# Optimization experiments

Hardware: AMD Instinct MI355X
Metric: run time of the kernel (lower is better)

The kernel has to match this reference:

```python
import jax, jax.numpy as jnp
import numpy as np

B, S, D = 4, 4096, 1024
DFF = 4 * D
ACTIVE = 1024  # ceil(S * 0.25)


def setup_inputs() -> dict:
    key = jax.random.key(0)
    ks = jax.random.split(key, 4)
    x = jax.random.normal(ks[0], (B, S, D), dtype=jnp.float32)
    rw = jax.random.normal(ks[1], (D,), dtype=jnp.float32) * 0.02
    rb = jnp.zeros((1,), dtype=jnp.float32)
    w1 = jax.random.normal(ks[2], (D, DFF), dtype=jnp.float32) * 0.02
    b1 = jnp.zeros((DFF,), dtype=jnp.float32)
    w2 = jax.random.normal(ks[3], (DFF, D), dtype=jnp.float32) * 0.02
    b2 = jnp.zeros((D,), dtype=jnp.float32)
    return {"x": x, "rw": rw, "rb": rb, "w1": w1, "b1": b1,
            "w2": w2, "b2": b2, "active_tokens": ACTIVE}


def reference(x, rw, rb, w1, b1, w2, b2, active_tokens):
    b, s, d = x.shape
    # router: Linear(n_embd, 1) -> [B, S] scores
    scores = jnp.einsum('bsd,d->bs', x, rw) + rb[0]
    # top-k tokens per batch row
    _, idx = jax.lax.top_k(scores, active_tokens)          # [B, K] int32
    sel = jnp.take_along_axis(x, idx[..., None], axis=1)   # [B, K, D]
    # dense MLP on selected tokens (exact GELU as in torch nn.GELU)
    h = jax.nn.gelu(jnp.einsum('bkd,df->bkf', sel, w1) + b1, approximate=False)
    out = jnp.einsum('bkf,fd->bkd', h, w2) + b2            # [B, K, D]
    # sigmoid gate from router scores of selected tokens
    gates = jax.nn.sigmoid(jnp.take_along_axis(scores, idx, axis=1))  # [B, K]
    out = out * gates[..., None]
    # scatter back into zeros at selected positions
    flat_idx = (idx + jnp.arange(b, dtype=idx.dtype)[:, None] * s).reshape(-1)
    flat_out = jnp.zeros((b * s, d), dtype=out.dtype)
    flat_out = flat_out.at[flat_idx].set(out.reshape(-1, d))
    return flat_out.reshape(b, s, d)
```

## Files before the change

### kernel.cpp

```cpp
#include <hip/hip_runtime.h>
#include <hip/hip_bf16.h>
#include <cstdint>
#include <cstddef>

#define Bz 4
#define Sz 4096
#define Dz 1024
#define DFFz 4096
#define KACT 1024

typedef __bf16 bf16;
typedef __attribute__((ext_vector_type(8))) __bf16 bf16x8;
typedef __attribute__((ext_vector_type(4))) __bf16 bf16x4;
typedef __attribute__((ext_vector_type(4))) float f32x4;

__device__ __forceinline__ void async16(const void* g, void* l) {
  __builtin_amdgcn_global_load_lds(
      (const __attribute__((address_space(1))) void*)g,
      (__attribute__((address_space(3))) void*)l, 16, 0, 0);
}

__global__ void router_k(const float* __restrict__ x, const float* __restrict__ rw,
                         const float* __restrict__ rb, float* __restrict__ scores,
                         float4* __restrict__ out4) {
  int row = blockIdx.x * 4 + (threadIdx.x >> 6);
  int lane = threadIdx.x & 63;
  const float4* xr = (const float4*)(x + (size_t)row * Dz);
  const float4* wr = (const float4*)rw;
  float acc = 0.f;
#pragma unroll
  for (int i = 0; i < 4; ++i) {
    float4 a = xr[lane + i * 64];
    float4 w = wr[lane + i * 64];
    acc += a.x * w.x + a.y * w.y + a.z * w.z + a.w * w.w;
  }
#pragma unroll
  for (int d = 32; d; d >>= 1) acc += __shfl_down(acc, d, 64);
  if (lane == 0) scores[row] = acc + rb[0];
  float4* o = out4 + (size_t)blockIdx.x * 4 * (Dz / 4);
  const float4 z = make_float4(0.f, 0.f, 0.f, 0.f);
#pragma unroll
  for (int i = 0; i < 4; ++i) o[threadIdx.x + i * 256] = z;
}

__global__ void transpose_cvt(const float* __restrict__ in, bf16* __restrict__ out,
                              int R, int C) {
  __shared__ float t[32][33];
  int c0 = blockIdx.x * 32, r0 = blockIdx.y * 32;
  int tx = threadIdx.x, ty = threadIdx.y;
#pragma unroll
  for (int i = 0; i < 32; i += 8) t[ty + i][tx] = in[(size_t)(r0 + ty + i) * C + c0 + tx];
  __syncthreads();
#pragma unroll
  for (int i = 0; i < 32; i += 8)
    out[(size_t)(c0 + ty + i) * R + r0 + tx] = (bf16)t[tx][ty + i];
}

__global__ __launch_bounds__(256) void select_gather_k(
    const float* __restrict__ x, const float* __restrict__ scores,
    int* __restrict__ sel_idx, float* __restrict__ gates, bf16* __restrict__ Xsel) {
  int b = blockIdx.x >> 8;
  int s0 = (blockIdx.x & 255) * 16;
  __shared__ float sc[Sz];
  __shared__ int red[16][4];
  __shared__ int rk[16];
  const int tid = threadIdx.x;
  const int wave = tid >> 6, lane = tid & 63;
  const float* srow = scores + (size_t)b * Sz;
#pragma unroll
  for (int i = 0; i < 4; ++i)
    ((float4*)sc)[tid + i * 256] = ((const float4*)srow)[tid + i * 256];
  __syncthreads();
  float mine[16];
#pragma unroll
  for (int j = 0; j < 16; ++j) mine[j] = sc[s0 + j];
  int cnt[16] = {};
  for (int t = tid; t < Sz; t += 256) {
    float o = sc[t];
#pragma unroll
    for (int j = 0; j < 16; ++j)
      cnt[j] += (o > mine[j]) || (o == mine[j] && t < s0 + j);
  }
#pragma unroll
  for (int j = 0; j < 16; ++j) {
    int c = cnt[j];
#pragma unroll
    for (int d = 32; d; d >>= 1) c += __shfl_down(c, d, 64);
    if (lane == 0) red[j][wave] = c;
  }
  __syncthreads();
  if (tid < 16) {
    int rank = red[tid][0] + red[tid][1] + red[tid][2] + red[tid][3];
    rk[tid] = rank;
    if (rank < KACT) {
      int m = b * KACT + rank;
      sel_idx[m] = s0 + tid;
      gates[m] = 1.f / (1.f + expf(-sc[s0 + tid]));
    }
  }
  __syncthreads();
#pragma unroll
  for (int j = 0; j < 16; ++j) {
    int rank = rk[j];
    if (rank >= KACT) continue;
    int m = b * KACT + rank;
    float4 v = ((const float4*)(x + ((size_t)b * Sz + s0 + j) * Dz))[tid];
    bf16x4 o = {(bf16)v.x, (bf16)v.y, (bf16)v.z, (bf16)v.w};
    ((bf16x4*)(Xsel + (size_t)m * Dz))[tid] = o;
  }
}

__global__ __launch_bounds__(256) void gemm1_k(const bf16* __restrict__ A,
                                               const bf16* __restrict__ Bt,
                                               const float* __restrict__ bias,
                                               bf16* __restrict__ H) {
  constexpr int K = Dz, N = DFFz;
  __shared__ __align__(16) bf16 As[128 * 32];
  __shared__ __align__(16) bf16 Bs[128 * 32];
  const int tid = threadIdx.x;
  const int wave = tid >> 6, lane = tid & 63;
  const int quad = lane >> 4, l16 = lane & 15;
  const int m0 = blockIdx.y * 128, n0 = blockIdx.x * 128;
  const int wm = (wave >> 1) * 64, wn = (wave & 1) * 64;
  const int r0 = tid >> 2;
  const int kk = (tid & 3) * 8;

  f32x4 acc[4][4] = {};

  const bf16* Ag = A + (size_t)(m0 + r0) * K + kk;
  const bf16* Bg = Bt + (size_t)(n0 + r0) * K + kk;
  bf16* lAs0 = &As[wave * 512];
  bf16* lAs1 = &As[2048 + wave * 512];
  bf16* lBs0 = &Bs[wave * 512];
  bf16* lBs1 = &Bs[2048 + wave * 512];

  for (int k0 = 0; k0 < K; k0 += 32) {
    async16(Ag + k0, lAs0);
    async16(Ag + (size_t)64 * K + k0, lAs1);
    async16(Bg + k0, lBs0);
    async16(Bg + (size_t)64 * K + k0, lBs1);
    __syncthreads();
    bf16x8 af[4], bfr[4];
#pragma unroll
    for (int i = 0; i < 4; ++i) {
      af[i] = *(const bf16x8*)&As[(wm + i * 16 + l16) * 32 + quad * 8];
      bfr[i] = *(const bf16x8*)&Bs[(wn + i * 16 + l16) * 32 + quad * 8];
    }
#pragma unroll
    for (int mi = 0; mi < 4; ++mi)
#pragma unroll
      for (int ni = 0; ni < 4; ++ni)
        acc[mi][ni] = __builtin_amdgcn_mfma_f32_16x16x32_bf16(af[mi], bfr[ni], acc[mi][ni], 0, 0, 0);
    __syncthreads();
  }

#pragma unroll
  for (int mi = 0; mi < 4; ++mi) {
    int mbase = m0 + wm + mi * 16 + quad * 4;
#pragma unroll
    for (int ni = 0; ni < 4; ++ni) {
      int n = n0 + wn + ni * 16 + l16;
      float bn = bias[n];
#pragma unroll
      for (int r = 0; r < 4; ++r) {
        float z = acc[mi][ni][r] + bn;
        float g = 0.5f * z * (1.f + erff(z * 0.70710678118654752f));
        H[(size_t)(mbase + r) * N + n] = (bf16)g;
      }
    }
  }
}

__global__ __launch_bounds__(256) void gemm2_k(const bf16* __restrict__ A,
                                               const bf16* __restrict__ Bt,
                                               const float* __restrict__ bias,
                                               const int* __restrict__ sel_idx,
                                               const float* __restrict__ gates,
                                               float* __restrict__ out) {
  constexpr int K = DFFz;
  __shared__ __align__(16) bf16 As[128 * 32];
  __shared__ __align__(16) bf16 Bs[64 * 32];
  const int tid = threadIdx.x;
  const int wave = tid >> 6, lane = tid & 63;
  const int quad = lane >> 4, l16 = lane & 15;
  const int m0 = blockIdx.y * 128, n0 = blockIdx.x * 64;
  const int wm = (wave >> 1) * 64, wn = (wave & 1) * 32;
  const int r0 = tid >> 2;
  const int kk = (tid & 3) * 8;

  f32x4 acc[4][2] = {};

  const bf16* Ag = A + (size_t)(m0 + r0) * K + kk;
  const bf16* Bg = Bt + (size_t)(n0 + r0) * K + kk;
  bf16* lAs0 = &As[wave * 512];
  bf16* lAs1 = &As[2048 + wave * 512];
  bf16* lBs0 = &Bs[wave * 512];

  for (int k0 = 0; k0 < K; k0 += 32) {
    async16(Ag + k0, lAs0);
    async16(Ag + (size_t)64 * K + k0, lAs1);
    async16(Bg + k0, lBs0);
    __syncthreads();
    bf16x8 af[4], bfr[2];
#pragma unroll
    for (int i = 0; i < 4; ++i)
      af[i] = *(const bf16x8*)&As[(wm + i * 16 + l16) * 32 + quad * 8];
#pragma unroll
    for (int j = 0; j < 2; ++j)
      bfr[j] = *(const bf16x8*)&Bs[(wn + j * 16 + l16) * 32 + quad * 8];
#pragma unroll
    for (int mi = 0; mi < 4; ++mi)
#pragma unroll
      for (int ni = 0; ni < 2; ++ni)
        acc[mi][ni] = __builtin_amdgcn_mfma_f32_16x16x32_bf16(af[mi], bfr[ni], acc[mi][ni], 0, 0, 0);
    __syncthreads();
  }

#pragma unroll
  for (int mi = 0; mi < 4; ++mi) {
#pragma unroll
    for (int r = 0; r < 4; ++r) {
      int m = m0 + wm + mi * 16 + quad * 4 + r;
      int b = m >> 10;
      int s = sel_idx[m];
      float gt = gates[m];
      float* orow = out + ((size_t)b * Sz + s) * Dz;
#pragma unroll
      for (int ni = 0; ni < 2; ++ni) {
        int n = n0 + wn + ni * 16 + l16;
        orow[n] = (acc[mi][ni][r] + bias[n]) * gt;
      }
    }
  }
}

extern "C" void kernel_launch(void* const* d_in, const int* in_sizes, int n_in,
                              void* d_out, int out_size, void* d_ws, size_t ws_size,
                              hipStream_t stream) {
  (void)in_sizes; (void)n_in; (void)out_size; (void)ws_size;
  const float* x  = (const float*)d_in[0];
  const float* rw = (const float*)d_in[1];
  const float* rb = (const float*)d_in[2];
  const float* w1 = (const float*)d_in[3];
  const float* b1 = (const float*)d_in[4];
  const float* w2 = (const float*)d_in[5];
  const float* b2 = (const float*)d_in[6];
  float* out = (float*)d_out;

  char* ws = (char*)d_ws;
  float* scores = (float*)ws;  ws += (size_t)Bz * Sz * 4;
  int*   sel_idx = (int*)ws;   ws += (size_t)Bz * KACT * 4;
  float* gates = (float*)ws;   ws += (size_t)Bz * KACT * 4;
  bf16*  w1T = (bf16*)ws;      ws += (size_t)DFFz * Dz * 2;
  bf16*  w2T = (bf16*)ws;      ws += (size_t)Dz * DFFz * 2;
  bf16*  Xsel = (bf16*)ws;     ws += (size_t)Bz * KACT * Dz * 2;
  bf16*  H = (bf16*)ws;        ws += (size_t)Bz * KACT * DFFz * 2;

  router_k<<<(Bz * Sz) / 4, 256, 0, stream>>>(x, rw, rb, scores, (float4*)out);
  transpose_cvt<<<dim3(DFFz / 32, Dz / 32), dim3(32, 8), 0, stream>>>(w1, w1T, Dz, DFFz);
  transpose_cvt<<<dim3(Dz / 32, DFFz / 32), dim3(32, 8), 0, stream>>>(w2, w2T, DFFz, Dz);
  select_gather_k<<<Bz * (Sz / 16), 256, 0, stream>>>(x, scores, sel_idx, gates, Xsel);
  gemm1_k<<<dim3(DFFz / 128, (Bz * KACT) / 128), 256, 0, stream>>>(Xsel, w1T, b1, H);
  gemm2_k<<<dim3(Dz / 64, (Bz * KACT) / 128), 256, 0, stream>>>(H, w2T, b2, sel_idx, gates, out);
}
```

Baseline: 315.3 us.

## Use BK=64 double-chunk k-steps and split-K the second GEMM with reduce kernel

Both GEMMs now load two 32-wide k-chunks per barrier pair, halving the number of synchronizations per unit of K. The second GEMM switches from 128x64 to 128x128 tiles and splits K into two halves over a z-grid. It writes bf16 partials into the workspace region reused from w1T. A new reduce kernel sums the two partials, adds bias, applies the gate and scatters rows to the output. This trades an extra kernel launch, extra partial-buffer traffic and bf16 rounding of partials for better occupancy and reuse in gemm2.

```diff
diff --git a/kernel.cpp b/kernel.cpp
--- a/kernel.cpp
+++ b/kernel.cpp
@@ -110,13 +110,38 @@
   }
 }
 
+#define GEMM_BK64_STEP(k0)                                                     \
+  _Pragma("unroll")                                                            \
+  for (int h = 0; h < 2; ++h) {                                                \
+    async16(Ag + (k0) + h * 32, &As[h * 4096 + tid * 8]);                      \
+    async16(Ag + (size_t)64 * K + (k0) + h * 32, &As[h * 4096 + 2048 + tid * 8]); \
+    async16(Bg + (k0) + h * 32, &Bs[h * 4096 + tid * 8]);                      \
+    async16(Bg + (size_t)64 * K + (k0) + h * 32, &Bs[h * 4096 + 2048 + tid * 8]); \
+  }                                                                            \
+  __syncthreads();                                                             \
+  _Pragma("unroll")                                                            \
+  for (int h = 0; h < 2; ++h) {                                                \
+    bf16x8 af[4], bfr[4];                                                      \
+    _Pragma("unroll")                                                          \
+    for (int i = 0; i < 4; ++i) {                                              \
+      af[i] = *(const bf16x8*)&As[h * 4096 + (wm + i * 16 + l16) * 32 + quad * 8]; \
+      bfr[i] = *(const bf16x8*)&Bs[h * 4096 + (wn + i * 16 + l16) * 32 + quad * 8]; \
+    }                                                                          \
+    _Pragma("unroll")                                                          \
+    for (int mi = 0; mi < 4; ++mi)                                             \
+      _Pragma("unroll")                                                        \
+      for (int ni = 0; ni < 4; ++ni)                                           \
+        acc[mi][ni] = __builtin_amdgcn_mfma_f32_16x16x32_bf16(af[mi], bfr[ni], acc[mi][ni], 0, 0, 0); \
+  }                                                                            \
+  __syncthreads();
+
 __global__ __launch_bounds__(256) void gemm1_k(const bf16* __restrict__ A,
                                                const bf16* __restrict__ Bt,
                                                const float* __restrict__ bias,
                                                bf16* __restrict__ H) {
   constexpr int K = Dz, N = DFFz;
-  __shared__ __align__(16) bf16 As[128 * 32];
-  __shared__ __align__(16) bf16 Bs[128 * 32];
+  __shared__ __align__(16) bf16 As[2 * 128 * 32];
+  __shared__ __align__(16) bf16 Bs[2 * 128 * 32];
   const int tid = threadIdx.x;
   const int wave = tid >> 6, lane = tid & 63;
   const int quad = lane >> 4, l16 = lane & 15;
@@ -124,34 +149,12 @@
   const int wm = (wave >> 1) * 64, wn = (wave & 1) * 64;
   const int r0 = tid >> 2;
   const int kk = (tid & 3) * 8;
-
   f32x4 acc[4][4] = {};
-
   const bf16* Ag = A + (size_t)(m0 + r0) * K + kk;
   const bf16* Bg = Bt + (size_t)(n0 + r0) * K + kk;
-  bf16* lAs0 = &As[wave * 512];
-  bf16* lAs1 = &As[2048 + wave * 512];
-  bf16* lBs0 = &Bs[wave * 512];
-  bf16* lBs1 = &Bs[2048 + wave * 512];
-
-  for (int k0 = 0; k0 < K; k0 += 32) {
-    async16(Ag + k0, lAs0);
-    async16(Ag + (size_t)64 * K + k0, lAs1);
-    async16(Bg + k0, lBs0);
-    async16(Bg + (size_t)64 * K + k0, lBs1);
-    __syncthreads();
-    bf16x8 af[4], bfr[4];
-#pragma unroll
-    for (int i = 0; i < 4; ++i) {
-      af[i] = *(const bf16x8*)&As[(wm + i * 16 + l16) * 32 + quad * 8];
-      bfr[i] = *(const bf16x8*)&Bs[(wn + i * 16 + l16) * 32 + quad * 8];
-    }
-#pragma unroll
-    for (int mi = 0; mi < 4; ++mi)
-#pragma unroll
-      for (int ni = 0; ni < 4; ++ni)
-        acc[mi][ni] = __builtin_amdgcn_mfma_f32_16x16x32_bf16(af[mi], bfr[ni], acc[mi][ni], 0, 0, 0);
-    __syncthreads();
+
+  for (int k0 = 0; k0 < K; k0 += 64) {
+    GEMM_BK64_STEP(k0)
   }
 
 #pragma unroll
@@ -173,65 +176,62 @@
 
 __global__ __launch_bounds__(256) void gemm2_k(const bf16* __restrict__ A,
                                                const bf16* __restrict__ Bt,
-                                               const float* __restrict__ bias,
-                                               const int* __restrict__ sel_idx,
-                                               const float* __restrict__ gates,
-                                               float* __restrict__ out) {
+                                               bf16* __restrict__ P) {
   constexpr int K = DFFz;
-  __shared__ __align__(16) bf16 As[128 * 32];
-  __shared__ __align__(16) bf16 Bs[64 * 32];
+  __shared__ __align__(16) bf16 As[2 * 128 * 32];
+  __shared__ __align__(16) bf16 Bs[2 * 128 * 32];
   const int tid = threadIdx.x;
   const int wave = tid >> 6, lane = tid & 63;
   const int quad = lane >> 4, l16 = lane & 15;
-  const int m0 = blockIdx.y * 128, n0 = blockIdx.x * 64;
-  const int wm = (wave >> 1) * 64, wn = (wave & 1) * 32;
+  const int m0 = blockIdx.y * 128, n0 = blockIdx.x * 128;
+  const int kc0 = blockIdx.z * 2048;
+  const int wm = (wave >> 1) * 64, wn = (wave & 1) * 64;
   const int r0 = tid >> 2;
   const int kk = (tid & 3) * 8;
-
-  f32x4 acc[4][2] = {};
-
-  const bf16* Ag = A + (size_t)(m0 + r0) * K + kk;
-  const bf16* Bg = Bt + (size_t)(n0 + r0) * K + kk;
-  bf16* lAs0 = &As[wave * 512];
-  bf16* lAs1 = &As[2048 + wave * 512];
-  bf16* lBs0 = &Bs[wave * 512];
-
-  for (int k0 = 0; k0 < K; k0 += 32) {
-    async16(Ag + k0, lAs0);
-    async16(Ag + (size_t)64 * K + k0, lAs1);
-    async16(Bg + k0, lBs0);
-    __syncthreads();
-    bf16x8 af[4], bfr[2];
-#pragma unroll
-    for (int i = 0; i < 4; ++i)
-      af[i] = *(const bf16x8*)&As[(wm + i * 16 + l16) * 32 + quad * 8];
-#pragma unroll
-    for (int j = 0; j < 2; ++j)
-      bfr[j] = *(const bf16x8*)&Bs[(wn + j * 16 + l16) * 32 + quad * 8];
-#pragma unroll
-    for (int mi = 0; mi < 4; ++mi)
-#pragma unroll
-      for (int ni = 0; ni < 2; ++ni)
-        acc[mi][ni] = __builtin_amdgcn_mfma_f32_16x16x32_bf16(af[mi], bfr[ni], acc[mi][ni], 0, 0, 0);
-    __syncthreads();
-  }
-
+  f32x4 acc[4][4] = {};
+  const bf16* Ag = A + (size_t)(m0 + r0) * K + kc0 + kk;
+  const bf16* Bg = Bt + (size_t)(n0 + r0) * K + kc0 + kk;
+
+  for (int k0 = 0; k0 < 2048; k0 += 64) {
+    GEMM_BK64_STEP(k0)
+  }
+
+  bf16* Pc = P + (size_t)blockIdx.z * Bz * KACT * Dz;
 #pragma unroll
   for (int mi = 0; mi < 4; ++mi) {
-#pragma unroll
-    for (int r = 0; r < 4; ++r) {
-      int m = m0 + wm + mi * 16 + quad * 4 + r;
-      int b = m >> 10;
-      int s = sel_idx[m];
-      float gt = gates[m];
-      float* orow = out + ((size_t)b * Sz + s) * Dz;
-#pragma unroll
-      for (int ni = 0; ni < 2; ++ni) {
-        int n = n0 + wn + ni * 16 + l16;
-        orow[n] = (acc[mi][ni][r] + bias[n]) * gt;
-      }
+    int mbase = m0 + wm + mi * 16 + quad * 4;
+#pragma unroll
+    for (int ni = 0; ni < 4; ++ni) {
+      int n = n0 + wn + ni * 16 + l16;
+#pragma unroll
+      for (int r = 0; r < 4; ++r)
+        Pc[(size_t)(mbase + r) * Dz + n] = (bf16)acc[mi][ni][r];
     }
   }
+}
+
+__global__ __launch_bounds__(256) void reduce_k(const bf16* __restrict__ P,
+                                                const float* __restrict__ bias,
+                                                const int* __restrict__ sel_idx,
+                                                const float* __restrict__ gates,
+                                                float* __restrict__ out) {
+  int m = blockIdx.x;
+  int b = m >> 10;
+  int s = sel_idx[m];
+  float gt = gates[m];
+  int tid = threadIdx.x;
+  const bf16x4* p0 = (const bf16x4*)(P + (size_t)m * Dz);
+  const bf16x4* p1 = (const bf16x4*)(P + (size_t)Bz * KACT * Dz + (size_t)m * Dz);
+  const float4* bv = (const float4*)bias;
+  float4* orow = (float4*)(out + ((size_t)b * Sz + s) * Dz);
+  bf16x4 a = p0[tid], c = p1[tid];
+  float4 bb = bv[tid];
+  float4 o;
+  o.x = ((float)a[0] + (float)c[0] + bb.x) * gt;
+  o.y = ((float)a[1] + (float)c[1] + bb.y) * gt;
+  o.z = ((float)a[2] + (float)c[2] + bb.z) * gt;
+  o.w = ((float)a[3] + (float)c[3] + bb.w) * gt;
+  orow[tid] = o;
 }
 
 extern "C" void kernel_launch(void* const* d_in, const int* in_sizes, int n_in,
@@ -251,15 +251,17 @@
   float* scores = (float*)ws;  ws += (size_t)Bz * Sz * 4;
   int*   sel_idx = (int*)ws;   ws += (size_t)Bz * KACT * 4;
   float* gates = (float*)ws;   ws += (size_t)Bz * KACT * 4;
+  bf16*  w2T = (bf16*)ws;      ws += (size_t)Dz * DFFz * 2;
+  bf16*  H = (bf16*)ws;        ws += (size_t)Bz * KACT * DFFz * 2;
   bf16*  w1T = (bf16*)ws;      ws += (size_t)DFFz * Dz * 2;
-  bf16*  w2T = (bf16*)ws;      ws += (size_t)Dz * DFFz * 2;
   bf16*  Xsel = (bf16*)ws;     ws += (size_t)Bz * KACT * Dz * 2;
-  bf16*  H = (bf16*)ws;        ws += (size_t)Bz * KACT * DFFz * 2;
+  bf16*  P = w1T;
 
   router_k<<<(Bz * Sz) / 4, 256, 0, stream>>>(x, rw, rb, scores, (float4*)out);
   transpose_cvt<<<dim3(DFFz / 32, Dz / 32), dim3(32, 8), 0, stream>>>(w1, w1T, Dz, DFFz);
   transpose_cvt<<<dim3(Dz / 32, DFFz / 32), dim3(32, 8), 0, stream>>>(w2, w2T, DFFz, Dz);
   select_gather_k<<<Bz * (Sz / 16), 256, 0, stream>>>(x, scores, sel_idx, gates, Xsel);
   gemm1_k<<<dim3(DFFz / 128, (Bz * KACT) / 128), 256, 0, stream>>>(Xsel, w1T, b1, H);
-  gemm2_k<<<dim3(Dz / 64, (Bz * KACT) / 128), 256, 0, stream>>>(H, w2T, b2, sel_idx, gates, out);
-}
+  gemm2_k<<<dim3(Dz / 128, (Bz * KACT) / 128, 2), 256, 0, stream>>>(H, w2T, P);
+  reduce_k<<<Bz * KACT, 256, 0, stream>>>(P, b2, sel_idx, gates, out);
+}
```

New measurement: 299.3 us. -5.1%, faster.
